# Kernel optimization log

Hardware: AMD Instinct MI355X
Metric: run time of the kernel (lower is better)

## Reference

```python
import jax, jax.numpy as jnp
import numpy as np

K = 5        # spline kernel_size per dim (dim=2 -> 25 kernel weights)
NPG = 75     # MNIST superpixel nodes per graph


def _spline_conv(x, src, dst, pseudo, emask, W, root, bias):
    """SplineConv, dim=2, kernel_size=5, degree=1 open splines, aggr='mean'.
    emask in {0,1} masks out coalesced-away (duplicate/self-loop) edges."""
    n = x.shape[0]
    v = jnp.clip(pseudo, 0.0, 1.0) * (K - 1)
    bot = jnp.clip(jnp.floor(v), 0, K - 2)
    frac = v - bot                                   # [E,2]
    bot = bot.astype(jnp.int32)
    xj = x[src] * emask[:, None]                     # [E,Fin] gathered source feats
    # aggregate-then-transform: acc[k,i,:] = sum over edges into i with basis k
    acc = jnp.zeros((K * K, n, x.shape[1]), x.dtype)
    for o0 in (0, 1):
        for o1 in (0, 1):
            w = (frac[:, 0] if o0 else 1.0 - frac[:, 0]) * (frac[:, 1] if o1 else 1.0 - frac[:, 1])
            kk = (bot[:, 0] + o0) + K * (bot[:, 1] + o1)
            acc = acc.at[kk, dst].add(w[:, None] * xj)
    out = jnp.einsum('knf,kfo->no', acc, W)
    deg = jax.ops.segment_sum(emask, dst, num_segments=n)
    return out / jnp.maximum(deg, 1.0)[:, None] + x @ root + bias


def _pool(x, pos, valid, batch, src, dst, emask, size, G, B):
    """voxel_grid + max_pool with static shapes: S=B*G*G clusters, masked."""
    S = B * G * G
    c = jnp.clip(jnp.floor(pos / size).astype(jnp.int32), 0, G - 1)
    cl = batch * (G * G) + c[:, 1] * G + c[:, 0]
    xm = jnp.where(valid[:, None] > 0, x, -1e30)
    px = jax.ops.segment_max(xm, cl, num_segments=S)
    cnt = jax.ops.segment_sum(valid, cl, num_segments=S)
    sval = (cnt > 0).astype(x.dtype)
    px = jnp.where(sval[:, None] > 0, px, 0.0)
    ppos = jax.ops.segment_sum(pos * valid[:, None], cl, num_segments=S) / jnp.maximum(cnt, 1.0)[:, None]
    nb = jnp.arange(S, dtype=jnp.int32) // (G * G)
    # remap edges to clusters; mask self loops and duplicates (= coalesce)
    nsrc, ndst = cl[src], cl[dst]
    m = (emask > 0) & (nsrc != ndst)
    a0 = jnp.where(m, nsrc, S)
    b0 = jnp.where(m, ndst, S)
    order = jnp.lexsort((b0, a0))
    a, b = a0[order], b0[order]
    first = jnp.concatenate([jnp.array([True]), (a[1:] != a[:-1]) | (b[1:] != b[:-1])])
    keep = jnp.zeros(src.shape[0], dtype=bool).at[order].set(first & (a < S))
    kf = keep.astype(x.dtype)
    # T.Cartesian(cat=False, norm=True): pseudo = (pos_src-pos_dst)/(2*max|.|)+0.5
    cart = ppos[nsrc] - ppos[ndst]
    amax = jnp.maximum(jnp.max(jnp.abs(cart) * kf[:, None]), 1e-12)
    pseudo = cart / (2.0 * amax) + 0.5
    return px, ppos, sval, nb, nsrc, ndst, kf, pseudo


def _forward(x, pos, src, dst, W1, r1, b1, W2, r2, b2, W3, r3, b3, fw1, fb1, fw2, fb2):
    N = x.shape[0]
    B = N // NPG
    batch = jnp.arange(N, dtype=jnp.int32) // NPG
    valid = jnp.ones((N,), x.dtype)
    emask = jnp.ones((src.shape[0],), x.dtype)
    cart = pos[src] - pos[dst]
    pseudo = cart / (2.0 * jnp.maximum(jnp.max(jnp.abs(cart)), 1e-12)) + 0.5
    x = jax.nn.elu(_spline_conv(x, src, dst, pseudo, emask, W1, r1, b1))
    x, pos, valid, batch, src, dst, emask, pseudo = _pool(x, pos, valid, batch, src, dst, emask, 5.0, 6, B)
    x = jax.nn.elu(_spline_conv(x, src, dst, pseudo, emask, W2, r2, b2))
    x, pos, valid, batch, src, dst, emask, pseudo = _pool(x, pos, valid, batch, src, dst, emask, 7.0, 5, B)
    x = jax.nn.elu(_spline_conv(x, src, dst, pseudo, emask, W3, r3, b3))
    # max_pool_x(cluster, x, batch, size=4): 2x2 voxel grid (size=14, end=27.99)
    c = jnp.clip(jnp.floor(pos / 14.0).astype(jnp.int32), 0, 1)
    cl = batch * 4 + c[:, 1] * 2 + c[:, 0]
    xm = jnp.where(valid[:, None] > 0, x, -1e30)
    px = jax.ops.segment_max(xm, cl, num_segments=B * 4)
    cnt = jax.ops.segment_sum(valid, cl, num_segments=B * 4)
    px = jnp.where((cnt > 0)[:, None], px, 0.0)
    h = jax.nn.elu(px.reshape(B, 4 * 64) @ fw1.T + fb1)
    logits = h @ fw2.T + fb2  # F.dropout is identity in eval mode
    return jax.nn.log_softmax(logits, axis=1)


def setup_inputs() -> dict:
    key = jax.random.key(0)
    ks = jax.random.split(key, 16)
    B, EPG = 1024, 1392
    N = B * NPG
    x = jax.random.normal(ks[0], (N, 1), jnp.float32)
    pos = jax.random.uniform(ks[1], (N, 2), jnp.float32) * 27.99
    s = jax.random.randint(ks[2], (B, EPG), 0, NPG)
    d = (s + 1 + jax.random.randint(ks[3], (B, EPG), 0, NPG - 1)) % NPG  # no self loops
    off = (jnp.arange(B, dtype=jnp.int32) * NPG)[:, None]
    src = (s + off).reshape(-1)
    dst = (d + off).reshape(-1)
    rn = lambda k, sh, sc: jax.random.normal(k, sh, jnp.float32) * sc
    return dict(x=x, pos=pos, src=src, dst=dst,
                W1=rn(ks[4], (25, 1, 32), 0.2), r1=rn(ks[5], (1, 32), 0.2), b1=jnp.zeros((32,), jnp.float32),
                W2=rn(ks[6], (25, 32, 64), 0.05), r2=rn(ks[7], (32, 64), 0.1), b2=jnp.zeros((64,), jnp.float32),
                W3=rn(ks[8], (25, 64, 64), 0.04), r3=rn(ks[9], (64, 64), 0.08), b3=jnp.zeros((64,), jnp.float32),
                fw1=rn(ks[10], (128, 256), 0.06), fb1=jnp.zeros((128,), jnp.float32),
                fw2=rn(ks[11], (10, 128), 0.09), fb2=jnp.zeros((10,), jnp.float32))


def reference(x, pos, src, dst, W1, r1, b1, W2, r2, b2, W3, r3, b3, fw1, fb1, fw2, fb2):
    return _forward(x, pos, src, dst, W1, r1, b1, W2, r2, b2, W3, r3, b3, fw1, fb1, fw2, fb2)
```

## Files before the change

kernel.cpp:

```cpp
#include <hip/hip_runtime.h>
#include <math.h>

#define NPG 75
#define KDIM 5

typedef _Float16 half8 __attribute__((ext_vector_type(8)));
typedef _Float16 half4 __attribute__((ext_vector_type(4)));
typedef float f32x4 __attribute__((ext_vector_type(4)));

__device__ __forceinline__ float eluf(float v){ return v > 0.f ? v : expf(v) - 1.f; }

__device__ __forceinline__ unsigned fenc(float f){
    unsigned u = __float_as_uint(f);
    return (u & 0x80000000u) ? ~u : (u | 0x80000000u);
}
__device__ __forceinline__ float fdec(unsigned u){
    return (u & 0x80000000u) ? __uint_as_float(u & 0x7FFFFFFFu) : __uint_as_float(~u);
}

__device__ __forceinline__ void fma25(float (&r)[25], const float (&wx)[5], const float (&wyx)[5]){
    #pragma unroll
    for (int b1 = 0; b1 < 5; b1++)
        #pragma unroll
        for (int b0 = 0; b0 < 5; b0++)
            asm("v_fmac_f32 %0, %1, %2" : "+v"(r[b1 * 5 + b0]) : "v"(wx[b0]), "v"(wyx[b1]));
}

__device__ __forceinline__ void spline2(float c0, float c1, float am, int* kks, float* wsp){
    float denom = 2.f * fmaxf(am, 1e-12f);
    float p0 = c0 / denom + 0.5f;
    float p1 = c1 / denom + 0.5f;
    p0 = fminf(fmaxf(p0, 0.f), 1.f) * 4.f;
    p1 = fminf(fmaxf(p1, 0.f), 1.f) * 4.f;
    float b0 = fminf(floorf(p0), 3.f);
    float b1 = fminf(floorf(p1), 3.f);
    float f0 = p0 - b0, f1 = p1 - b1;
    int i0 = (int)b0, i1 = (int)b1;
    wsp[0] = (1.f - f0) * (1.f - f1); kks[0] = i0     + KDIM *  i1;
    wsp[1] =        f0  * (1.f - f1); kks[1] = i0 + 1 + KDIM *  i1;
    wsp[2] = (1.f - f0) *        f1 ; kks[2] = i0     + KDIM * (i1 + 1);
    wsp[3] =        f0  *        f1 ; kks[3] = i0 + 1 + KDIM * (i1 + 1);
}

__global__ __launch_bounds__(256) void amax0_k(
        const float* __restrict__ pos, const int* __restrict__ src,
        const int* __restrict__ dst, int E4, unsigned* __restrict__ outbits){
    float cand = 0.f;
    for (int i = blockIdx.x * 256 + threadIdx.x; i < E4; i += gridDim.x * 256){
        int4 s4 = ((const int4*)src)[i];
        int4 d4 = ((const int4*)dst)[i];
        #pragma unroll
        for (int k = 0; k < 4; k++){
            int s = (&s4.x)[k], d = (&d4.x)[k];
            float c0 = pos[s*2]   - pos[d*2];
            float c1 = pos[s*2+1] - pos[d*2+1];
            cand = fmaxf(cand, fmaxf(fabsf(c0), fabsf(c1)));
        }
    }
    __shared__ float sm[256];
    sm[threadIdx.x] = cand; __syncthreads();
    for (int o = 128; o > 0; o >>= 1){
        if (threadIdx.x < o) sm[threadIdx.x] = fmaxf(sm[threadIdx.x], sm[threadIdx.x + o]);
        __syncthreads();
    }
    if (threadIdx.x == 0) atomicMax(outbits, __float_as_uint(sm[0]));
}

__global__ __launch_bounds__(512) void conv1pool1_k(
        const float* __restrict__ x, const float* __restrict__ pos,
        const int* __restrict__ src, const int* __restrict__ dst, int EPG,
        const unsigned* __restrict__ amaxp,
        const float* __restrict__ W1, const float* __restrict__ r1, const float* __restrict__ b1,
        float* __restrict__ px1, float* __restrict__ pp1, float* __restrict__ sv1,
        int* __restrict__ cl1){
    __shared__ __align__(16) float acc[NPG * 28];
    __shared__ float deg[NPG];
    __shared__ float xl[NPG], p0l[NPG], p1l[NPG];
    __shared__ int   cli[NPG];
    __shared__ float W1s[800], r1s[32], b1s[32];
    __shared__ unsigned px[36 * 32];
    __shared__ float cnt[36], ps[72];

    const int b = blockIdx.x, t = threadIdx.x;
    const int n0 = b * NPG, e0 = b * EPG;

    const float am = __uint_as_float(*amaxp);

    for (int i = t; i < NPG * 28; i += 512) acc[i] = 0.f;
    for (int i = t; i < 36 * 32; i += 512) px[i] = 0u;
    if (t < NPG) deg[t] = 0.f;
    if (t < 36) cnt[t] = 0.f;
    if (t < 72) ps[t] = 0.f;
    for (int i = t; i < 800; i += 512) W1s[i] = W1[i];
    if (t < 32){ r1s[t] = r1[t]; b1s[t] = b1[t]; }
    if (t < NPG){
        float p0 = pos[(n0 + t) * 2], p1 = pos[(n0 + t) * 2 + 1];
        xl[t] = x[n0 + t]; p0l[t] = p0; p1l[t] = p1;
        int c0 = min(max((int)floorf(p0 / 5.f), 0), 5);
        int c1 = min(max((int)floorf(p1 / 5.f), 0), 5);
        int c = c1 * 6 + c0;
        cli[t] = c;
        cl1[n0 + t] = b * 36 + c;
    }
    __syncthreads();

    const int o = t & 31;
    float wreg[25];
    #pragma unroll
    for (int k = 0; k < 25; k++) wreg[k] = W1s[k * 32 + o];
    const float rro = r1s[o], bbo = b1s[o];

    if (t < NPG){
        int c = cli[t];
        atomicAdd(&cnt[c], 1.f);
        atomicAdd(&ps[c*2],     p0l[t]);
        atomicAdd(&ps[c*2 + 1], p1l[t]);
    }

    for (int e = t; e < EPG; e += 512){
        int s = src[e0 + e] - n0;
        int d = dst[e0 + e] - n0;
        float c0 = p0l[s] - p0l[d];
        float c1 = p1l[s] - p1l[d];
        int kks[4]; float wsp[4];
        spline2(c0, c1, am, kks, wsp);
        float xv = xl[s];
        #pragma unroll
        for (int c = 0; c < 4; c++) atomicAdd(&acc[d*28 + kks[c]], wsp[c] * xv);
        atomicAdd(&deg[d], 1.f);
    }
    __syncthreads();

    const int ii = t >> 5;
    #pragma unroll
    for (int r = 0; r < 5; r++){
        int i = ii + r * 16;
        if (i < NPG){
            const float4* ar = (const float4*)(acc + i * 28);
            float s = 0.f;
            #pragma unroll
            for (int q = 0; q < 7; q++){
                float4 aq = ar[q];
                s += aq.x * wreg[q*4];
                if (q*4 + 1 < 25) s += aq.y * wreg[q*4 + 1];
                if (q*4 + 2 < 25) s += aq.z * wreg[q*4 + 2];
                if (q*4 + 3 < 25) s += aq.w * wreg[q*4 + 3];
            }
            float v = s / fmaxf(deg[i], 1.f) + xl[i] * rro + bbo;
            v = eluf(v);
            atomicMax(&px[cli[i]*32 + o], fenc(v));
        }
    }
    __syncthreads();

    for (int idx = t; idx < 36 * 32; idx += 512){
        int s_ = idx >> 5;
        px1[(size_t)(b*36)*32 + idx] = (cnt[s_] > 0.f) ? fdec(px[idx]) : 0.f;
    }
    if (t < 36){
        float c = cnt[t], m = fmaxf(c, 1.f);
        pp1[(b*36 + t)*2]     = ps[t*2] / m;
        pp1[(b*36 + t)*2 + 1] = ps[t*2 + 1] / m;
        sv1[b*36 + t] = (c > 0.f) ? 1.f : 0.f;
    }
}

template<int GG, int NN>
__global__ __launch_bounds__(1024) void dedup_csr_k(
        const int* src_in, const int* dst_in,
        const int* __restrict__ clmap, const unsigned char* __restrict__ kf_in,
        unsigned char* kf_out, int* es_out, int* ed_out,
        const float* __restrict__ pp, int EPG,
        int* __restrict__ easrc, float2* __restrict__ ecart,
        int* __restrict__ rowptr2, int* __restrict__ kcnt, unsigned* __restrict__ amaxbits){
    __shared__ unsigned pm[GG * GG];
    __shared__ float degs[GG];
    __shared__ int rs[GG + 1];
    __shared__ int cur[GG];
    __shared__ float red[16];
    __shared__ int   clS[NN];
    __shared__ float ppS[2 * GG];

    const int b = blockIdx.x, t = threadIdx.x;
    const int lane = t & 63, wid = t >> 6;
    const int e0 = b * EPG;
    const int cbase = b * GG;

    for (int i = t; i < GG * GG; i += 1024) pm[i] = 0xFFFFFFFFu;
    if (t < GG) degs[t] = 0.f;
    if (t < NN) clS[t] = clmap[b * NN + t] - cbase;
    if (t < 2 * GG) ppS[t] = pp[cbase * 2 + t];
    __syncthreads();

    const int niter = (EPG + 1023) / 1024;
    int la[2], lb[2]; bool lm[2];
    const int nbase = b * NN;
    for (int it = 0; it < niter; it++){
        int e = t + it * 1024;
        lm[it] = false;
        if (e < EPG){
            int a  = clS[src_in[e0 + e] - nbase];
            int bb = clS[dst_in[e0 + e] - nbase];
            la[it] = a; lb[it] = bb;
            es_out[e0 + e] = cbase + a; ed_out[e0 + e] = cbase + bb;
            bool m = (kf_in ? (kf_in[e0 + e] != 0) : true) && (a != bb);
            lm[it] = m;
            if (m) atomicMin(&pm[a * GG + bb], (unsigned)e);
        }
    }
    __syncthreads();

    float cand = 0.f;
    bool kept[2]; float lc0[2], lc1[2];
    for (int it = 0; it < niter; it++){
        int e = t + it * 1024;
        kept[it] = false;
        if (e < EPG){
            bool k = false;
            if (lm[it]) k = (pm[la[it] * GG + lb[it]] == (unsigned)e);
            kept[it] = k;
            if (kf_out) kf_out[e0 + e] = k ? 1 : 0;
            if (k){
                atomicAdd(&degs[lb[it]], 1.f);
                float c0 = ppS[la[it]*2]     - ppS[lb[it]*2];
                float c1 = ppS[la[it]*2 + 1] - ppS[lb[it]*2 + 1];
                lc0[it] = c0; lc1[it] = c1;
                cand = fmaxf(cand, fmaxf(fabsf(c0), fabsf(c1)));
            }
        }
    }
    #pragma unroll
    for (int o = 1; o < 64; o <<= 1) cand = fmaxf(cand, __shfl_xor(cand, o, 64));
    if (lane == 0) red[wid] = cand;
    __syncthreads();
    if (t == 0){
        float m = red[0];
        #pragma unroll
        for (int i = 1; i < 16; i++) m = fmaxf(m, red[i]);
        atomicMax(amaxbits, __float_as_uint(m));
    }
    if (t < 64){
        int v = (t < GG) ? (int)degs[t] : 0;
        int incl = v;
        #pragma unroll
        for (int o = 1; o < 64; o <<= 1){
            int u = __shfl_up(incl, o, 64);
            if (t >= o) incl += u;
        }
        if (t == 0) rs[0] = 0;
        if (t < GG) rs[t + 1] = incl;
    }
    __syncthreads();
    if (t < GG){
        rowptr2[(cbase + t)*2]     = e0 + rs[t];
        rowptr2[(cbase + t)*2 + 1] = e0 + rs[t + 1];
        cur[t] = rs[t];
    }
    if (t == 0) kcnt[b] = rs[GG];
    __syncthreads();
    for (int it = 0; it < niter; it++){
        if (kept[it]){
            int slot = atomicAdd(&cur[lb[it]], 1);
            easrc[e0 + slot] = cbase + la[it];
            ecart[e0 + slot] = make_float2(lc0[it], lc1[it]);
        }
    }
}

__global__ __launch_bounds__(1024) void dedup_pool_k(
        const int* __restrict__ src_in, const int* __restrict__ dst_in,
        const unsigned char* __restrict__ kf_in,
        const float* __restrict__ xin,
        const float* __restrict__ pp1, const float* __restrict__ sv1,
        int EPG,
        float* __restrict__ px2, float* __restrict__ pp2, float* __restrict__ sv2,
        int* __restrict__ easrc, float2* __restrict__ ecart,
        int* __restrict__ rowptr2, int* __restrict__ kcnt, unsigned* __restrict__ amaxbits){
    constexpr int GG = 25, NN = 36;
    __shared__ unsigned pm[GG * GG];
    __shared__ float degs[GG];
    __shared__ int rs[GG + 1];
    __shared__ int cur[GG];
    __shared__ float red[16];
    __shared__ int   clS[NN];
    __shared__ int   vld[NN];
    __shared__ float ppS[2 * GG];
    __shared__ unsigned px[GG * 64];
    __shared__ float cnt[GG], ps[2 * GG];

    const int b = blockIdx.x, t = threadIdx.x;
    const int lane = t & 63, wid = t >> 6;
    const int e0 = b * EPG;
    const int cbase = b * GG;
    const int nb36  = b * NN;

    for (int i = t; i < GG * GG; i += 1024) pm[i] = 0xFFFFFFFFu;
    for (int i = t; i < GG * 64; i += 1024) px[i] = 0u;
    if (t < GG){ degs[t] = 0.f; cnt[t] = 0.f; }
    if (t < 2 * GG) ps[t] = 0.f;
    if (t < NN){
        float v  = sv1[nb36 + t];
        float p0 = pp1[(nb36 + t)*2], p1 = pp1[(nb36 + t)*2 + 1];
        int c0 = min(max((int)floorf(p0 / 7.f), 0), 4);
        int c1 = min(max((int)floorf(p1 / 7.f), 0), 4);
        clS[t] = c1 * 5 + c0;
        vld[t] = (v > 0.f) ? 1 : 0;
    }
    __syncthreads();

    if (t < NN && vld[t]){
        int c = clS[t];
        atomicAdd(&cnt[c], 1.f);
        atomicAdd(&ps[c*2],     pp1[(nb36 + t)*2]);
        atomicAdd(&ps[c*2 + 1], pp1[(nb36 + t)*2 + 1]);
    }
    for (int idx = t; idx < NN * 64; idx += 1024){
        int i = idx >> 6, f = idx & 63;
        if (vld[i])
            atomicMax(&px[clS[i]*64 + f], fenc(xin[(size_t)(nb36 + i)*64 + f]));
    }
    const int niter = (EPG + 1023) / 1024;
    int la[2], lb[2]; bool lm[2];
    for (int it = 0; it < niter; it++){
        int e = t + it * 1024;
        lm[it] = false;
        if (e < EPG){
            int a  = clS[src_in[e0 + e] - nb36];
            int bb = clS[dst_in[e0 + e] - nb36];
            la[it] = a; lb[it] = bb;
            bool m = (kf_in[e0 + e] != 0) && (a != bb);
            lm[it] = m;
            if (m) atomicMin(&pm[a * GG + bb], (unsigned)e);
        }
    }
    __syncthreads();

    if (t < GG){
        float c = cnt[t], m = fmaxf(c, 1.f);
        float q0 = ps[t*2] / m, q1 = ps[t*2 + 1] / m;
        ppS[t*2] = q0; ppS[t*2 + 1] = q1;
        pp2[(cbase + t)*2]     = q0;
        pp2[(cbase + t)*2 + 1] = q1;
        sv2[cbase + t] = (c > 0.f) ? 1.f : 0.f;
    }
    for (int idx = t; idx < GG * 64; idx += 1024){
        int s_ = idx >> 6;
        px2[(size_t)cbase*64 + idx] = (cnt[s_] > 0.f) ? fdec(px[idx]) : 0.f;
    }
    __syncthreads();

    float cand = 0.f;
    bool kept[2]; float lc0[2], lc1[2];
    for (int it = 0; it < niter; it++){
        int e = t + it * 1024;
        kept[it] = false;
        if (e < EPG){
            bool k = false;
            if (lm[it]) k = (pm[la[it] * GG + lb[it]] == (unsigned)e);
            kept[it] = k;
            if (k){
                atomicAdd(&degs[lb[it]], 1.f);
                float c0 = ppS[la[it]*2]     - ppS[lb[it]*2];
                float c1 = ppS[la[it]*2 + 1] - ppS[lb[it]*2 + 1];
                lc0[it] = c0; lc1[it] = c1;
                cand = fmaxf(cand, fmaxf(fabsf(c0), fabsf(c1)));
            }
        }
    }
    #pragma unroll
    for (int o = 1; o < 64; o <<= 1) cand = fmaxf(cand, __shfl_xor(cand, o, 64));
    if (lane == 0) red[wid] = cand;
    __syncthreads();
    if (t == 0){
        float m = red[0];
        #pragma unroll
        for (int i = 1; i < 16; i++) m = fmaxf(m, red[i]);
        atomicMax(amaxbits, __float_as_uint(m));
    }
    if (t < 64){
        int v = (t < GG) ? (int)degs[t] : 0;
        int incl = v;
        #pragma unroll
        for (int o = 1; o < 64; o <<= 1){
            int u = __shfl_up(incl, o, 64);
            if (t >= o) incl += u;
        }
        if (t == 0) rs[0] = 0;
        if (t < GG) rs[t + 1] = incl;
    }
    __syncthreads();
    if (t < GG){
        rowptr2[(cbase + t)*2]     = e0 + rs[t];
        rowptr2[(cbase + t)*2 + 1] = e0 + rs[t + 1];
        cur[t] = rs[t];
    }
    if (t == 0) kcnt[b] = rs[GG];
    __syncthreads();
    for (int it = 0; it < niter; it++){
        if (kept[it]){
            int slot = atomicAdd(&cur[lb[it]], 1);
            easrc[e0 + slot] = cbase + la[it];
            ecart[e0 + slot] = make_float2(lc0[it], lc1[it]);
        }
    }
}

__global__ void wswz2_k(const float* __restrict__ W2, const float* __restrict__ r2,
                        const float* __restrict__ W3, const float* __restrict__ r3,
                        _Float16* __restrict__ Wz2, _Float16* __restrict__ Wz3){
    int gid = blockIdx.x * 256 + threadIdx.x;
    const int T2 = 26 * 32 * 64;
    const int T3 = 26 * 64 * 64;
    const float* W; const float* root; _Float16* Wz; int FIN; int g;
    if (gid < T2){ W = W2; root = r2; Wz = Wz2; FIN = 32; g = gid; }
    else if (gid < T2 + T3){ W = W3; root = r3; Wz = Wz3; FIN = 64; g = gid - T2; }
    else return;
    int k = g >> 6, n = g & 63;
    float v = (k < 25 * FIN) ? W[(size_t)k * 64 + n] : root[(size_t)(k - 25 * FIN) * 64 + n];
    int kt = k >> 5, kr = k & 31, quad = kr >> 3, j = kr & 7;
    int lane = (quad << 4) | (n & 15);
    int nt = n >> 4;
    Wz[(((size_t)(kt * 4 + nt) * 64 + lane) << 3) + j] = (_Float16)v;
}

template<int FIN>
__global__ __launch_bounds__(64) void conv_gather_k(
        const float* __restrict__ x, const int* __restrict__ easrc,
        const float2* __restrict__ ecart, const unsigned* __restrict__ amaxp,
        const int* __restrict__ rowptr2, _Float16* __restrict__ Aout){
    constexpr int KTOT = 26 * FIN;
    const int lane = threadIdx.x;
    const int node = blockIdx.x;
    const int row0 = rowptr2[node*2], row1 = rowptr2[node*2 + 1];
    constexpr int STEP = (FIN == 32) ? 2 : 1;
    const int sub = (FIN == 32) ? (lane >> 5) : 0;
    const int f = lane & (FIN - 1);

    const float am = __uint_as_float(*amaxp);
    const float denom = 2.f * fmaxf(am, 1e-12f);

    float r[25];
    #pragma unroll
    for (int b = 0; b < 25; b++) r[b] = 0.f;

    int iCur = row0 + sub;
    int aNext = 0;
    float2 ccC = make_float2(0.f, 0.f);
    float xvCur = 0.f;
    if (iCur < row1){
        int aCur = easrc[iCur];
        ccC = ecart[iCur];
        xvCur = x[(size_t)aCur * FIN + f];
        int i1 = (iCur + STEP < row1) ? iCur + STEP : iCur;
        aNext = easrc[i1];
    }
    for (; iCur < row1; iCur += STEP){
        int iN  = iCur + STEP;
        int iNs = (iN < row1) ? iN : iCur;
        int iN2 = (iN + STEP < row1) ? iN + STEP : iNs;
        float2 ccN = ecart[iNs];
        float xvN = x[(size_t)aNext * FIN + f];
        int aN2 = easrc[iN2];
        float p0 = fminf(fmaxf(ccC.x / denom + 0.5f, 0.f), 1.f) * 4.f;
        float p1 = fminf(fmaxf(ccC.y / denom + 0.5f, 0.f), 1.f) * 4.f;
        float b0 = fminf(floorf(p0), 3.f);
        float b1 = fminf(floorf(p1), 3.f);
        int i0 = (int)b0, i1 = (int)b1;
        float f0 = p0 - b0, f1 = p1 - b1;
        float wx[5], wyx[5];
        #pragma unroll
        for (int k = 0; k < 5; k++){
            wx[k] = (k == i0) ? (1.f - f0) : ((k == i0 + 1) ? f0 : 0.f);
            float wy = (k == i1) ? (1.f - f1) : ((k == i1 + 1) ? f1 : 0.f);
            wyx[k] = wy * xvCur;
        }
        fma25(r, wx, wyx);
        ccC = ccN; xvCur = xvN; aNext = aN2;
    }

    if (FIN == 32){
        #pragma unroll
        for (int b = 0; b < 25; b++) r[b] += __shfl_xor(r[b], 32, 64);
    }

    float inv = 1.f / (float)max(row1 - row0, 1);
    _Float16* dstrow = Aout + (size_t)node * KTOT;
    if (FIN == 64){
        #pragma unroll
        for (int b = 0; b < 25; b++) dstrow[b * 64 + f] = (_Float16)(r[b] * inv);
        dstrow[25 * 64 + f] = (_Float16)x[(size_t)node * 64 + f];
    } else {
        #pragma unroll
        for (int b = 0; b < 25; b++)
            if ((b & 1) == sub) dstrow[b * 32 + f] = (_Float16)(r[b] * inv);
        if (sub == 0) dstrow[25 * 32 + f] = (_Float16)x[(size_t)node * 32 + f];
    }
}

template<int KTOT>
__global__ __launch_bounds__(256) void conv_mfma_k(
        const _Float16* __restrict__ A, const _Float16* __restrict__ Wz,
        const float* __restrict__ bias, int M, float* __restrict__ out){
    constexpr int NSTEP = KTOT / 32;
    const int w = threadIdx.x >> 6, lane = threadIdx.x & 63;
    const int m0 = blockIdx.x * 64 + w * 16;
    const int quad = lane >> 4;

    f32x4 acc[4];
    #pragma unroll
    for (int nt = 0; nt < 4; nt++) acc[nt] = (f32x4){0.f, 0.f, 0.f, 0.f};

    const half8* __restrict__ Arow = (const half8*)(A + (size_t)(m0 + (lane & 15)) * KTOT);
    const half8* __restrict__ Wp   = (const half8*)Wz + lane;

    for (int kt = 0; kt < NSTEP; kt++){
        half8 a = Arow[kt * 4 + quad];
        #pragma unroll
        for (int nt = 0; nt < 4; nt++){
            half8 b = Wp[(kt * 4 + nt) * 64];
            acc[nt] = __builtin_amdgcn_mfma_f32_16x16x32_f16(a, b, acc[nt], 0, 0, 0);
        }
    }

    float* cp = out + (size_t)m0 * 64;
    const int r = quad * 4, c = lane & 15;
    #pragma unroll
    for (int nt = 0; nt < 4; nt++){
        float bv = bias[nt * 16 + c];
        #pragma unroll
        for (int i = 0; i < 4; i++)
            cp[(size_t)(r + i) * 64 + nt * 16 + c] = eluf(acc[nt][i] + bv);
    }
}

__global__ __launch_bounds__(256) void final_k(
        const float* __restrict__ xin, const float* __restrict__ ppin,
        const float* __restrict__ svin,
        const float* __restrict__ fw1, const float* __restrict__ fb1,
        const float* __restrict__ fw2, const float* __restrict__ fb2,
        float* __restrict__ out){
    __shared__ unsigned px[4 * 64];
    __shared__ float cnt[4];
    __shared__ int cli[25];
    __shared__ float xr[256];
    __shared__ float h[128];
    __shared__ float lg[10];
    __shared__ float lse;
    const int b = blockIdx.x, t = threadIdx.x;

    if (t < 4*64) px[t] = 0u;
    if (t < 4) cnt[t] = 0.f;
    if (t < 25){
        float v  = svin[b*25 + t];
        float p0 = ppin[(b*25 + t)*2], p1 = ppin[(b*25 + t)*2 + 1];
        int c0 = min(max((int)floorf(p0 / 14.f), 0), 1);
        int c1 = min(max((int)floorf(p1 / 14.f), 0), 1);
        int c = c1 * 2 + c0;
        cli[t] = (v > 0.f) ? c : -1;
    }
    __syncthreads();
    if (t < 25 && cli[t] >= 0) atomicAdd(&cnt[cli[t]], 1.f);
    __syncthreads();
    for (int idx = t; idx < 25 * 64; idx += 256){
        int i = idx >> 6, f = idx & 63;
        if (cli[i] >= 0)
            atomicMax(&px[cli[i]*64 + f], fenc(xin[(size_t)(b*25 + i)*64 + f]));
    }
    __syncthreads();
    xr[t] = (cnt[t >> 6] > 0.f) ? fdec(px[t]) : 0.f;
    __syncthreads();
    if (t < 128){
        float s = fb1[t];
        const float4* wrow = (const float4*)(fw1 + (size_t)t * 256);
        #pragma unroll 4
        for (int i = 0; i < 64; i++){
            float4 q = wrow[i];
            s += xr[i*4]   * q.x;
            s += xr[i*4+1] * q.y;
            s += xr[i*4+2] * q.z;
            s += xr[i*4+3] * q.w;
        }
        h[t] = eluf(s);
    }
    __syncthreads();
    if (t < 10){
        float s2 = fb2[t];
        const float* w2 = fw2 + (size_t)t * 128;
        for (int j = 0; j < 128; j++) s2 += h[j] * w2[j];
        lg[t] = s2;
    }
    __syncthreads();
    if (t == 0){
        float m = lg[0];
        for (int c = 1; c < 10; c++) m = fmaxf(m, lg[c]);
        float se = 0.f;
        for (int c = 0; c < 10; c++) se += expf(lg[c] - m);
        lse = m + logf(se);
    }
    __syncthreads();
    if (t < 10) out[(size_t)b*10 + t] = lg[t] - lse;
}

extern "C" void kernel_launch(void* const* d_in, const int* in_sizes, int n_in,
                              void* d_out, int out_size, void* d_ws, size_t ws_size,
                              hipStream_t stream) {
    const float* x   = (const float*)d_in[0];
    const float* pos = (const float*)d_in[1];
    const int*   src = (const int*)d_in[2];
    const int*   dst = (const int*)d_in[3];
    const float* W1  = (const float*)d_in[4];
    const float* r1  = (const float*)d_in[5];
    const float* b1  = (const float*)d_in[6];
    const float* W2  = (const float*)d_in[7];
    const float* r2  = (const float*)d_in[8];
    const float* b2  = (const float*)d_in[9];
    const float* W3  = (const float*)d_in[10];
    const float* r3  = (const float*)d_in[11];
    const float* b3  = (const float*)d_in[12];
    const float* fw1 = (const float*)d_in[13];
    const float* fb1 = (const float*)d_in[14];
    const float* fw2 = (const float*)d_in[15];
    const float* fb2 = (const float*)d_in[16];
    float* out = (float*)d_out;

    const int N   = in_sizes[0];
    const int E   = in_sizes[2];
    const int B   = N / NPG;
    const int EPG = E / B;
    const int S1  = B * 36;
    const int S2  = B * 25;

    float* w = (float*)d_ws;
    size_t off = 0;
    auto alloc = [&](size_t nelem){ size_t o = off; off += (nelem + 63) & ~(size_t)63; return o; };

    size_t o_scal = alloc(4);
    size_t o_px1  = alloc((size_t)S1 * 32);
    size_t o_pp1  = alloc((size_t)S1 * 2);
    size_t o_sv1  = alloc(S1);
    size_t o_cl1  = alloc(N);
    size_t o_kf1  = alloc((E + 3) / 4);
    size_t o_es1  = alloc(E);
    size_t o_ed1  = alloc(E);
    size_t o_easrc= alloc(E);
    size_t o_ecart= alloc((size_t)2 * E);
    size_t o_kcnt = alloc(B);
    size_t o_rp2  = alloc((size_t)2 * S1);
    size_t o_rp3  = alloc((size_t)2 * S2);
    size_t o_out2 = alloc((size_t)S1 * 64);
    size_t o_px2  = alloc((size_t)S2 * 64);
    size_t o_pp2  = alloc((size_t)S2 * 2);
    size_t o_sv2  = alloc(S2);
    size_t o_out3 = alloc((size_t)S2 * 64);
    size_t o_wz2  = alloc((size_t)26 * 32 * 64 / 2 + 64);
    size_t o_wz3  = alloc((size_t)26 * 64 * 64 / 2 + 64);
    size_t accAhalfs = (size_t)S1 * 832 > (size_t)S2 * 1664 ? (size_t)S1 * 832 : (size_t)S2 * 1664;
    size_t o_accA = alloc((accAhalfs + 1) / 2);

    hipMemsetAsync(w + o_scal, 0, 4 * sizeof(float), stream);

    unsigned* scal = (unsigned*)(w + o_scal);
    _Float16* Wz2  = (_Float16*)(w + o_wz2);
    _Float16* Wz3  = (_Float16*)(w + o_wz3);
    _Float16* A16  = (_Float16*)(w + o_accA);
    auto nb = [](long long t){ return (unsigned)((t + 255) / 256); };

    wswz2_k<<<nb(26 * 32 * 64 + 26 * 64 * 64), 256, 0, stream>>>(W2, r2, W3, r3, Wz2, Wz3);

    const int E4 = E / 4;
    int gA = (E4 + 255) / 256; if (gA > 512) gA = 512;
    amax0_k<<<gA, 256, 0, stream>>>(pos, src, dst, E4, scal + 0);
    conv1pool1_k<<<B, 512, 0, stream>>>(x, pos, src, dst, EPG, scal + 0, W1, r1, b1,
                                        w + o_px1, w + o_pp1, w + o_sv1, (int*)(w + o_cl1));

    dedup_csr_k<36, NPG><<<B, 1024, 0, stream>>>(
        src, dst, (int*)(w + o_cl1), nullptr,
        (unsigned char*)(w + o_kf1), (int*)(w + o_es1), (int*)(w + o_ed1),
        w + o_pp1, EPG, (int*)(w + o_easrc), (float2*)(w + o_ecart),
        (int*)(w + o_rp2), (int*)(w + o_kcnt), scal + 1);

    conv_gather_k<32><<<S1, 64, 0, stream>>>(
        w + o_px1, (int*)(w + o_easrc), (const float2*)(w + o_ecart), scal + 1,
        (int*)(w + o_rp2), A16);
    conv_mfma_k<832><<<S1 / 64, 256, 0, stream>>>(A16, Wz2, b2, S1, w + o_out2);

    dedup_pool_k<<<B, 1024, 0, stream>>>(
        (int*)(w + o_es1), (int*)(w + o_ed1), (unsigned char*)(w + o_kf1),
        w + o_out2, w + o_pp1, w + o_sv1, EPG,
        w + o_px2, w + o_pp2, w + o_sv2,
        (int*)(w + o_easrc), (float2*)(w + o_ecart),
        (int*)(w + o_rp3), (int*)(w + o_kcnt), scal + 2);

    conv_gather_k<64><<<S2, 64, 0, stream>>>(
        w + o_px2, (int*)(w + o_easrc), (const float2*)(w + o_ecart), scal + 2,
        (int*)(w + o_rp3), A16);
    conv_mfma_k<1664><<<S2 / 64, 256, 0, stream>>>(A16, Wz3, b3, S2, w + o_out3);

    final_k<<<B, 256, 0, stream>>>(w + o_out3, w + o_pp2, w + o_sv2,
                                   fw1, fb1, fw2, fb2, out);
}
```

Baseline: 380.4 us.

## Precompute per-edge spline basis weights in a separate kernel and pack four nodes per block

Adds an espline_k kernel that computes each edge's open-spline basis weights once and stores them as 8 floats. The gather kernel then reads these weights instead of recomputing them in every lane; the fifth weight is recovered as one minus the sum of the other four. The gather kernel also now handles four nodes per 256-thread block instead of one node per 64-thread block. The cost is two extra kernel launches and 32 bytes of extra memory traffic per edge, in exchange for less redundant ALU work per feature lane.

Result: faster. 359.8 us (-5.4%).

```diff
diff --git a/kernel.cpp b/kernel.cpp
--- a/kernel.cpp
+++ b/kernel.cpp
@@ -405,6 +405,33 @@
     }
 }
 
+__global__ void espline_k(const float2* __restrict__ ecart, const unsigned* __restrict__ amaxp,
+                          const int* __restrict__ kcnt, int EPG, int E,
+                          float* __restrict__ edata){
+    int i = blockIdx.x * 256 + threadIdx.x;
+    if (i >= E) return;
+    int b = i / EPG;
+    if (i - b * EPG >= kcnt[b]) return;
+    float2 c = ecart[i];
+    float am = __uint_as_float(*amaxp);
+    float denom = 2.f * fmaxf(am, 1e-12f);
+    float p0 = fminf(fmaxf(c.x / denom + 0.5f, 0.f), 1.f) * 4.f;
+    float p1 = fminf(fmaxf(c.y / denom + 0.5f, 0.f), 1.f) * 4.f;
+    float b0 = fminf(floorf(p0), 3.f);
+    float b1 = fminf(floorf(p1), 3.f);
+    int i0 = (int)b0, i1 = (int)b1;
+    float f0 = p0 - b0, f1 = p1 - b1;
+    float wx[5], wy[5];
+    #pragma unroll
+    for (int k = 0; k < 5; k++){
+        wx[k] = (k == i0) ? (1.f - f0) : ((k == i0 + 1) ? f0 : 0.f);
+        wy[k] = (k == i1) ? (1.f - f1) : ((k == i1 + 1) ? f1 : 0.f);
+    }
+    float* d = edata + (size_t)i * 8;
+    *(float4*)(d)     = make_float4(wx[0], wx[1], wx[2], wx[3]);
+    *(float4*)(d + 4) = make_float4(wy[0], wy[1], wy[2], wy[3]);
+}
+
 __global__ void wswz2_k(const float* __restrict__ W2, const float* __restrict__ r2,
                         const float* __restrict__ W3, const float* __restrict__ r3,
                         _Float16* __restrict__ Wz2, _Float16* __restrict__ Wz3){
@@ -424,32 +451,30 @@
 }
 
 template<int FIN>
-__global__ __launch_bounds__(64) void conv_gather_k(
+__global__ __launch_bounds__(256) void conv_gather_k(
         const float* __restrict__ x, const int* __restrict__ easrc,
-        const float2* __restrict__ ecart, const unsigned* __restrict__ amaxp,
+        const float* __restrict__ edata,
         const int* __restrict__ rowptr2, _Float16* __restrict__ Aout){
     constexpr int KTOT = 26 * FIN;
-    const int lane = threadIdx.x;
-    const int node = blockIdx.x;
+    const int lane = threadIdx.x & 63;
+    const int node = blockIdx.x * 4 + (threadIdx.x >> 6);
     const int row0 = rowptr2[node*2], row1 = rowptr2[node*2 + 1];
     constexpr int STEP = (FIN == 32) ? 2 : 1;
     const int sub = (FIN == 32) ? (lane >> 5) : 0;
     const int f = lane & (FIN - 1);
 
-    const float am = __uint_as_float(*amaxp);
-    const float denom = 2.f * fmaxf(am, 1e-12f);
-
     float r[25];
     #pragma unroll
     for (int b = 0; b < 25; b++) r[b] = 0.f;
 
     int iCur = row0 + sub;
     int aNext = 0;
-    float2 ccC = make_float2(0.f, 0.f);
+    float4 waC, wbC;
     float xvCur = 0.f;
     if (iCur < row1){
         int aCur = easrc[iCur];
-        ccC = ecart[iCur];
+        const float* d = edata + (size_t)iCur * 8;
+        waC = *(const float4*)(d); wbC = *(const float4*)(d + 4);
         xvCur = x[(size_t)aCur * FIN + f];
         int i1 = (iCur + STEP < row1) ? iCur + STEP : iCur;
         aNext = easrc[i1];
@@ -458,24 +483,17 @@
         int iN  = iCur + STEP;
         int iNs = (iN < row1) ? iN : iCur;
         int iN2 = (iN + STEP < row1) ? iN + STEP : iNs;
-        float2 ccN = ecart[iNs];
+        const float* dn = edata + (size_t)iNs * 8;
+        float4 waN = *(const float4*)(dn);
+        float4 wbN = *(const float4*)(dn + 4);
         float xvN = x[(size_t)aNext * FIN + f];
         int aN2 = easrc[iN2];
-        float p0 = fminf(fmaxf(ccC.x / denom + 0.5f, 0.f), 1.f) * 4.f;
-        float p1 = fminf(fmaxf(ccC.y / denom + 0.5f, 0.f), 1.f) * 4.f;
-        float b0 = fminf(floorf(p0), 3.f);
-        float b1 = fminf(floorf(p1), 3.f);
-        int i0 = (int)b0, i1 = (int)b1;
-        float f0 = p0 - b0, f1 = p1 - b1;
-        float wx[5], wyx[5];
-        #pragma unroll
-        for (int k = 0; k < 5; k++){
-            wx[k] = (k == i0) ? (1.f - f0) : ((k == i0 + 1) ? f0 : 0.f);
-            float wy = (k == i1) ? (1.f - f1) : ((k == i1 + 1) ? f1 : 0.f);
-            wyx[k] = wy * xvCur;
-        }
+        float wx4 = 1.f - (waC.x + waC.y + waC.z + waC.w);
+        float wy4 = 1.f - (wbC.x + wbC.y + wbC.z + wbC.w);
+        float wx[5]  = {waC.x, waC.y, waC.z, waC.w, wx4};
+        float wyx[5] = {wbC.x * xvCur, wbC.y * xvCur, wbC.z * xvCur, wbC.w * xvCur, wy4 * xvCur};
         fma25(r, wx, wyx);
-        ccC = ccN; xvCur = xvN; aNext = aN2;
+        waC = waN; wbC = wbN; xvCur = xvN; aNext = aN2;
     }
 
     if (FIN == 32){
@@ -644,6 +662,7 @@
     size_t o_ed1  = alloc(E);
     size_t o_easrc= alloc(E);
     size_t o_ecart= alloc((size_t)2 * E);
+    size_t o_edat = alloc((size_t)8 * E);
     size_t o_kcnt = alloc(B);
     size_t o_rp2  = alloc((size_t)2 * S1);
     size_t o_rp3  = alloc((size_t)2 * S2);
@@ -678,9 +697,11 @@
         (unsigned char*)(w + o_kf1), (int*)(w + o_es1), (int*)(w + o_ed1),
         w + o_pp1, EPG, (int*)(w + o_easrc), (float2*)(w + o_ecart),
         (int*)(w + o_rp2), (int*)(w + o_kcnt), scal + 1);
-
-    conv_gather_k<32><<<S1, 64, 0, stream>>>(
-        w + o_px1, (int*)(w + o_easrc), (const float2*)(w + o_ecart), scal + 1,
+    espline_k<<<nb(E), 256, 0, stream>>>((float2*)(w + o_ecart), scal + 1,
+                                         (int*)(w + o_kcnt), EPG, E, w + o_edat);
+
+    conv_gather_k<32><<<S1 / 4, 256, 0, stream>>>(
+        w + o_px1, (int*)(w + o_easrc), w + o_edat,
         (int*)(w + o_rp2), A16);
     conv_mfma_k<832><<<S1 / 64, 256, 0, stream>>>(A16, Wz2, b2, S1, w + o_out2);
 
@@ -690,9 +711,11 @@
         w + o_px2, w + o_pp2, w + o_sv2,
         (int*)(w + o_easrc), (float2*)(w + o_ecart),
         (int*)(w + o_rp3), (int*)(w + o_kcnt), scal + 2);
-
-    conv_gather_k<64><<<S2, 64, 0, stream>>>(
-        w + o_px2, (int*)(w + o_easrc), (const float2*)(w + o_ecart), scal + 2,
+    espline_k<<<nb(E), 256, 0, stream>>>((float2*)(w + o_ecart), scal + 2,
+                                         (int*)(w + o_kcnt), EPG, E, w + o_edat);
+
+    conv_gather_k<64><<<S2 / 4, 256, 0, stream>>>(
+        w + o_px2, (int*)(w + o_easrc), w + o_edat,
         (int*)(w + o_rp3), A16);
     conv_mfma_k<1664><<<S2 / 64, 256, 0, stream>>>(A16, Wz3, b3, S2, w + o_out3);
 
```
